# Kernel tuning notes

Hardware: AMD Instinct MI355X
Metric: run time of the kernel (lower is better)

Reference implementation:

```python
import jax, jax.numpy as jnp
import numpy as np

B, D_IN, H, D_OUT = 1024, 64, 128, 16


def setup_inputs() -> dict:
    key = jax.random.key(0)
    k0, k1, k2 = jax.random.split(key, 3)
    x = jax.random.normal(k0, (B, D_IN), dtype=jnp.float32)
    W1 = jax.random.normal(k1, (D_IN, H), dtype=jnp.float32) / np.sqrt(D_IN).astype(np.float32)
    b1 = jnp.zeros((H,), dtype=jnp.float32)
    W2 = jax.random.normal(k2, (H, D_OUT), dtype=jnp.float32) / np.sqrt(H).astype(np.float32)
    b2 = jnp.zeros((D_OUT,), dtype=jnp.float32)
    return {"x": x, "W1": W1, "b1": b1, "W2": W2, "b2": b2}


def reference(x, W1, b1, W2, b2):
    # Wrapped net: 2-layer tanh MLP (hessQuik NN equivalent).
    def f_single(xi):  # xi: [D_IN] -> [D_OUT]
        return jnp.tanh(xi @ W1 + b1) @ W2 + b2

    # f: [B, D_OUT]  (torch: f.view(B, -1))
    f = jax.vmap(f_single)(x)

    # Torch builds df[b, i, j] = d f_j / d x_i via one grad per output column;
    # one reverse sweep per output == jacrev, vmapped over batch.
    J = jax.vmap(jax.jacrev(f_single))(x)            # [B, D_OUT, D_IN]
    df = jnp.transpose(J, (0, 2, 1))                 # [B, D_IN, D_OUT]

    # Torch builds d2f[b, k, i, j] = d^2 f_j / (d x_k d x_i); symmetric in (k, i).
    Hs = jax.vmap(jax.hessian(f_single))(x)          # [B, D_OUT, D_IN, D_IN]
    d2f = jnp.transpose(Hs, (0, 2, 3, 1))            # [B, D_IN, D_IN, D_OUT]

    return f, df, d2f
```

## Files before the change

### kernel.cpp

```cpp
#include <hip/hip_runtime.h>
#include <hip/hip_bf16.h>


typedef unsigned short u16;
typedef short s8v __attribute__((ext_vector_type(8)));
typedef float f4v __attribute__((ext_vector_type(4)));

__device__ __forceinline__ u16 f2bf(float f){
  __hip_bfloat16 h = __float2bfloat16(f);
  return __builtin_bit_cast(u16, h);
}

__global__ __launch_bounds__(128) void k1_fdf(
    const float* __restrict__ x,  const float* __restrict__ W1, const float* __restrict__ b1,
    const float* __restrict__ W2, const float* __restrict__ b2,
    float* __restrict__ f_out, float* __restrict__ df_out,
    u16* __restrict__ U, u16* __restrict__ Gt)
{
  const int b   = blockIdx.x;
  const int tid = threadIdx.x;

  __shared__ float sx[64];
  __shared__ float s_a[128];
  __shared__ float s_sw2[128 * 16];

  {
    const int base = b * 512;
#pragma unroll
    for (int u = 0; u < 4; ++u){
      int idx = base + u*128 + tid;
      int r = idx >> 7, h = idx & 127;
      float w = W1[(r & 63)*128 + h] * W1[(r >> 6)*128 + h];
      U[idx] = f2bf(w);
    }
  }

  if (tid < 64) sx[tid] = x[b*64 + tid];
  __syncthreads();

  float z = b1[tid];
#pragma unroll 8
  for (int i = 0; i < 64; ++i) z += sx[i] * W1[i*128 + tid];
  float a = tanhf(z);
  float s = 1.0f - a*a;
  float t = -2.0f * a * s;
  s_a[tid] = a;
#pragma unroll
  for (int j = 0; j < 16; ++j){
    float w2 = W2[tid*16 + j];
    s_sw2[tid*16 + j] = s * w2;
    Gt[(b*16 + j)*128 + tid] = f2bf(t * w2);
  }
  __syncthreads();

  if (tid < 16){
    float acc = b2[tid];
    for (int h = 0; h < 128; ++h) acc += s_a[h] * W2[h*16 + tid];
    __builtin_nontemporal_store(acc, &f_out[b*16 + tid]);
  }

  const int i  = tid >> 1;
  const int j0 = (tid & 1) * 8;
  float acc[8] = {0,0,0,0,0,0,0,0};
  for (int h0 = 0; h0 < 128; h0 += 8){
    const float4* wp = (const float4*)&W1[i*128 + h0];
    float4 wa = wp[0], wb = wp[1];
    float wf[8] = {wa.x, wa.y, wa.z, wa.w, wb.x, wb.y, wb.z, wb.w};
#pragma unroll
    for (int hh = 0; hh < 8; ++hh){
      const float4* sp = (const float4*)&s_sw2[(h0 + hh)*16 + j0];
      float4 A = sp[0], Bv = sp[1];
      float w1 = wf[hh];
      acc[0] += w1*A.x;  acc[1] += w1*A.y;  acc[2] += w1*A.z;  acc[3] += w1*A.w;
      acc[4] += w1*Bv.x; acc[5] += w1*Bv.y; acc[6] += w1*Bv.z; acc[7] += w1*Bv.w;
    }
  }
  f4v v0 = {acc[0], acc[1], acc[2], acc[3]};
  f4v v1 = {acc[4], acc[5], acc[6], acc[7]};
  float* dp = &df_out[b*1024 + i*16 + j0];
  __builtin_nontemporal_store(v0, (f4v*)dp);
  __builtin_nontemporal_store(v1, (f4v*)(dp + 4));
}

__global__ __launch_bounds__(256) void k2_d2f(
    const u16* __restrict__ U, const u16* __restrict__ Gt, float* __restrict__ d2f)
{
  const int tid  = threadIdx.x;
  const int lane = tid & 63;
  const int wave = tid >> 6;
  const int n = lane & 15;
  const int q = lane >> 4;
  const int b0 = blockIdx.x * 4;
  const int mb = blockIdx.y;

  s8v bfrag[4][4];
#pragma unroll
  for (int s = 0; s < 4; ++s){
    const u16* gp = Gt + ((b0 + s)*16 + n)*128 + q*8;
#pragma unroll
    for (int ks = 0; ks < 4; ++ks)
      bfrag[s][ks] = *(const s8v*)(gp + ks*32);
  }

  const int R0 = mb*1024 + wave*256;
#pragma unroll 2
  for (int mt = 0; mt < 16; ++mt){
    const int rowbase = R0 + mt*16;
    const u16* ap = U + (rowbase + n)*128 + q*8;
    s8v afrag[4];
#pragma unroll
    for (int ks = 0; ks < 4; ++ks)
      afrag[ks] = *(const s8v*)(ap + ks*32);

#pragma unroll
    for (int s = 0; s < 4; ++s){
      f4v acc = {0.f, 0.f, 0.f, 0.f};
#pragma unroll
      for (int ks = 0; ks < 4; ++ks)
        acc = __builtin_amdgcn_mfma_f32_16x16x32_bf16(bfrag[s][ks], afrag[ks], acc, 0, 0, 0);
      float* op = d2f + (size_t)(b0 + s)*65536 + (size_t)(rowbase + n)*16 + q*4;
      __builtin_nontemporal_store(acc, (f4v*)op);
    }
  }
}

extern "C" void kernel_launch(void* const* d_in, const int* in_sizes, int n_in,
                              void* d_out, int out_size, void* d_ws, size_t ws_size,
                              hipStream_t stream)
{
  (void)in_sizes; (void)n_in; (void)out_size; (void)ws_size;
  const float* x  = (const float*)d_in[0];
  const float* W1 = (const float*)d_in[1];
  const float* b1 = (const float*)d_in[2];
  const float* W2 = (const float*)d_in[3];
  const float* b2 = (const float*)d_in[4];

  float* out     = (float*)d_out;
  float* f_out   = out;
  float* df_out  = out + 16384;
  float* d2f_out = out + 1064960;

  u16* U  = (u16*)d_ws;
  u16* Gt = U + 524288;

  k1_fdf<<<1024, 128, 0, stream>>>(x, W1, b1, W2, b2, f_out, df_out, U, Gt);
  k2_d2f<<<dim3(256, 4), 256, 0, stream>>>(U, Gt, d2f_out);
}
```

Baseline: 306.9 us.

## Fuse Hessian factor generation into d2f MFMA kernel, drop workspace round-trip

The d2f kernel now computes the tanh second-derivative factors and the W1 outer-product A fragments on the fly from W1 held in shared memory. This removes the bf16 U and Gt workspace buffers that were written by k1 and read back by k2. The grid drops to 2 row blocks of 2048 rows, and an XOR swizzle is applied to the shared G tile. In exchange each block redoes the hidden-layer matvec for its 4 samples and rebuilds the A fragments per tile, adding ALU work and about 42KB of LDS per block, which limits occupancy.

Result: faster. 298.9 us (-2.6%).

```diff
diff --git a/kernel.cpp b/kernel.cpp
--- a/kernel.cpp
+++ b/kernel.cpp
@@ -11,11 +11,105 @@
   return __builtin_bit_cast(u16, h);
 }
 
+#define W1S 132
+
+__global__ __launch_bounds__(256) void k2_fused(
+    const float* __restrict__ x, const float* __restrict__ W1, const float* __restrict__ b1,
+    const float* __restrict__ W2, float* __restrict__ d2f)
+{
+  const int tid  = threadIdx.x;
+  const int lane = tid & 63;
+  const int wave = tid >> 6;
+  const int n = lane & 15;
+  const int q = lane >> 4;
+  const int b0 = blockIdx.x * 4;
+  const int mb = blockIdx.y;
+
+  __shared__ float sW1[64 * W1S];
+  __shared__ u16   sG[4 * 2048];
+  __shared__ float sx[256];
+
+#pragma unroll
+  for (int v = 0; v < 8; ++v){
+    int idx = v*256 + tid;
+    int r = idx >> 5;
+    int c = (idx & 31) << 2;
+    *(f4v*)&sW1[r*W1S + c] = *(const f4v*)&W1[r*128 + c];
+  }
+  sx[tid] = x[b0*64 + tid];
+  __syncthreads();
+
+#pragma unroll
+  for (int it = 0; it < 2; ++it){
+    int idx = it*256 + tid;
+    int s = idx >> 7;
+    int h = idx & 127;
+    float z = b1[h];
+#pragma unroll 8
+    for (int i = 0; i < 64; ++i) z += sx[s*64 + i] * sW1[i*W1S + h];
+    float a = tanhf(z);
+    float t = -2.0f * a * (1.0f - a*a);
+    f4v w2r[4];
+#pragma unroll
+    for (int v2 = 0; v2 < 4; ++v2) w2r[v2] = *(const f4v*)&W2[h*16 + v2*4];
+#pragma unroll
+    for (int j = 0; j < 16; ++j){
+      int byte = (j*256 + h*2) ^ ((j & 7) << 4);
+      sG[s*2048 + (byte >> 1)] = f2bf(t * w2r[j >> 2][j & 3]);
+    }
+  }
+  __syncthreads();
+
+  s8v bfrag[4][4];
+#pragma unroll
+  for (int s = 0; s < 4; ++s){
+#pragma unroll
+    for (int ks = 0; ks < 4; ++ks){
+      int byte = (n*256 + q*16 + ks*64) ^ ((n & 7) << 4);
+      bfrag[s][ks] = *(const s8v*)&sG[s*2048 + (byte >> 1)];
+    }
+  }
+
+  const int R0 = mb*2048 + wave*512;
+#pragma unroll 2
+  for (int mt = 0; mt < 32; ++mt){
+    const int rowbase = R0 + mt*16;
+    const int r = rowbase + n;
+    const int i = r & 63;
+    const int k = r >> 6;
+    const float* wi = &sW1[i*W1S];
+    const float* wk = &sW1[k*W1S];
+    s8v afrag[4];
+#pragma unroll
+    for (int ks = 0; ks < 4; ++ks){
+      int c = q*8 + ks*32;
+      f4v ia = *(const f4v*)&wi[c];
+      f4v ib = *(const f4v*)&wi[c+4];
+      f4v ka = *(const f4v*)&wk[c];
+      f4v kb = *(const f4v*)&wk[c+4];
+      s8v av;
+#pragma unroll
+      for (int e = 0; e < 4; ++e) av[e]   = (short)f2bf(ia[e]*ka[e]);
+#pragma unroll
+      for (int e = 0; e < 4; ++e) av[4+e] = (short)f2bf(ib[e]*kb[e]);
+      afrag[ks] = av;
+    }
+#pragma unroll
+    for (int s = 0; s < 4; ++s){
+      f4v acc = {0.f, 0.f, 0.f, 0.f};
+#pragma unroll
+      for (int ks = 0; ks < 4; ++ks)
+        acc = __builtin_amdgcn_mfma_f32_16x16x32_bf16(bfrag[s][ks], afrag[ks], acc, 0, 0, 0);
+      float* op = d2f + (size_t)(b0 + s)*65536 + (size_t)(rowbase + n)*16 + q*4;
+      __builtin_nontemporal_store(acc, (f4v*)op);
+    }
+  }
+}
+
 __global__ __launch_bounds__(128) void k1_fdf(
     const float* __restrict__ x,  const float* __restrict__ W1, const float* __restrict__ b1,
     const float* __restrict__ W2, const float* __restrict__ b2,
-    float* __restrict__ f_out, float* __restrict__ df_out,
-    u16* __restrict__ U, u16* __restrict__ Gt)
+    float* __restrict__ f_out, float* __restrict__ df_out)
 {
   const int b   = blockIdx.x;
   const int tid = threadIdx.x;
@@ -23,17 +117,6 @@
   __shared__ float sx[64];
   __shared__ float s_a[128];
   __shared__ float s_sw2[128 * 16];
-
-  {
-    const int base = b * 512;
-#pragma unroll
-    for (int u = 0; u < 4; ++u){
-      int idx = base + u*128 + tid;
-      int r = idx >> 7, h = idx & 127;
-      float w = W1[(r & 63)*128 + h] * W1[(r >> 6)*128 + h];
-      U[idx] = f2bf(w);
-    }
-  }
 
   if (tid < 64) sx[tid] = x[b*64 + tid];
   __syncthreads();
@@ -43,14 +126,10 @@
   for (int i = 0; i < 64; ++i) z += sx[i] * W1[i*128 + tid];
   float a = tanhf(z);
   float s = 1.0f - a*a;
-  float t = -2.0f * a * s;
   s_a[tid] = a;
 #pragma unroll
-  for (int j = 0; j < 16; ++j){
-    float w2 = W2[tid*16 + j];
-    s_sw2[tid*16 + j] = s * w2;
-    Gt[(b*16 + j)*128 + tid] = f2bf(t * w2);
-  }
+  for (int j = 0; j < 16; ++j)
+    s_sw2[tid*16 + j] = s * W2[tid*16 + j];
   __syncthreads();
 
   if (tid < 16){
@@ -82,53 +161,11 @@
   __builtin_nontemporal_store(v1, (f4v*)(dp + 4));
 }
 
-__global__ __launch_bounds__(256) void k2_d2f(
-    const u16* __restrict__ U, const u16* __restrict__ Gt, float* __restrict__ d2f)
-{
-  const int tid  = threadIdx.x;
-  const int lane = tid & 63;
-  const int wave = tid >> 6;
-  const int n = lane & 15;
-  const int q = lane >> 4;
-  const int b0 = blockIdx.x * 4;
-  const int mb = blockIdx.y;
-
-  s8v bfrag[4][4];
-#pragma unroll
-  for (int s = 0; s < 4; ++s){
-    const u16* gp = Gt + ((b0 + s)*16 + n)*128 + q*8;
-#pragma unroll
-    for (int ks = 0; ks < 4; ++ks)
-      bfrag[s][ks] = *(const s8v*)(gp + ks*32);
-  }
-
-  const int R0 = mb*1024 + wave*256;
-#pragma unroll 2
-  for (int mt = 0; mt < 16; ++mt){
-    const int rowbase = R0 + mt*16;
-    const u16* ap = U + (rowbase + n)*128 + q*8;
-    s8v afrag[4];
-#pragma unroll
-    for (int ks = 0; ks < 4; ++ks)
-      afrag[ks] = *(const s8v*)(ap + ks*32);
-
-#pragma unroll
-    for (int s = 0; s < 4; ++s){
-      f4v acc = {0.f, 0.f, 0.f, 0.f};
-#pragma unroll
-      for (int ks = 0; ks < 4; ++ks)
-        acc = __builtin_amdgcn_mfma_f32_16x16x32_bf16(bfrag[s][ks], afrag[ks], acc, 0, 0, 0);
-      float* op = d2f + (size_t)(b0 + s)*65536 + (size_t)(rowbase + n)*16 + q*4;
-      __builtin_nontemporal_store(acc, (f4v*)op);
-    }
-  }
-}
-
 extern "C" void kernel_launch(void* const* d_in, const int* in_sizes, int n_in,
                               void* d_out, int out_size, void* d_ws, size_t ws_size,
                               hipStream_t stream)
 {
-  (void)in_sizes; (void)n_in; (void)out_size; (void)ws_size;
+  (void)in_sizes; (void)n_in; (void)out_size; (void)d_ws; (void)ws_size;
   const float* x  = (const float*)d_in[0];
   const float* W1 = (const float*)d_in[1];
   const float* b1 = (const float*)d_in[2];
@@ -140,9 +177,6 @@
   float* df_out  = out + 16384;
   float* d2f_out = out + 1064960;
 
-  u16* U  = (u16*)d_ws;
-  u16* Gt = U + 524288;
-
-  k1_fdf<<<1024, 128, 0, stream>>>(x, W1, b1, W2, b2, f_out, df_out, U, Gt);
-  k2_d2f<<<dim3(256, 4), 256, 0, stream>>>(U, Gt, d2f_out);
+  k2_fused<<<dim3(256, 2), 256, 0, stream>>>(x, W1, b1, W2, d2f_out);
+  k1_fdf<<<1024, 128, 0, stream>>>(x, W1, b1, W2, b2, f_out, df_out);
 }
```
